# Kernel tuning notes

Hardware: AMD Instinct MI355X
Metric: run time of the kernel (lower is better)

Reference implementation:

```python
import jax, jax.numpy as jnp
import numpy as np

N_NODES = 100000
N_EDGES = 600000
D = 128
BN_EPS = 1e-5


def setup_inputs() -> dict:
    key = jax.random.key(0)
    k1, k2, k3 = jax.random.split(key, 3)
    x = jax.random.normal(k1, (N_NODES, D), dtype=jnp.float32)
    edge_index = jax.random.randint(k2, (2, N_EDGES), 0, N_NODES, dtype=jnp.int64)
    # Linear(in=D, out=D): kaiming-uniform-ish init
    W = jax.random.normal(k3, (D, D), dtype=jnp.float32) / np.sqrt(D)
    b = jnp.zeros((D,), dtype=jnp.float32)
    eps_gin = jnp.zeros((), dtype=jnp.float32)  # train_eps=True, init 0
    gamma = jnp.ones((D,), dtype=jnp.float32)
    beta = jnp.zeros((D,), dtype=jnp.float32)
    return {"x": x, "edge_index": edge_index, "W": W, "b": b,
            "eps_gin": eps_gin, "gamma": gamma, "beta": beta}


def reference(x, edge_index, W, b, eps_gin, gamma, beta):
    src, dst = edge_index[0], edge_index[1]
    # GIN aggregation: sum of source features into destination nodes
    agg = jax.ops.segment_sum(x[src], dst, num_segments=N_NODES)  # [N, D]
    h = (1.0 + eps_gin) * x + agg
    # MLP([D, D]) == single Linear (PyG plain_last)
    h = jnp.einsum('nd,df->nf', h, W.T) + b  # torch Linear: h @ W^T + b
    # BatchNorm1d in training mode (batch stats, biased variance)
    mean = jnp.mean(h, axis=0)
    var = jnp.mean((h - mean) ** 2, axis=0)
    h = (h - mean) * jax.lax.rsqrt(var + BN_EPS) * gamma + beta
    h = jax.nn.relu(h)
    # residual
    return h + x
```

## Files before the change

kernel.cpp:

```cpp
#include <hip/hip_runtime.h>
#include <hip/hip_bf16.h>

#define N_NODES 100000
#define N_EDGES 600000
#define D 128
#define BN_EPS 1e-5f
#define CAP 32
#define NAGG_BLOCKS 1024
#define GEMM_BLOCKS 1024
#define GEMM_NSLOTS (GEMM_BLOCKS * 2)
#define FILL_BLOCKS ((N_EDGES + 255) / 256)

typedef __bf16 bf16x8 __attribute__((ext_vector_type(8)));
typedef float floatx4 __attribute__((ext_vector_type(4)));
typedef unsigned short ushortx8 __attribute__((ext_vector_type(8)));

__device__ __forceinline__ unsigned short f2bf(float f) {
    union { float f; unsigned u; } v; v.f = f;
    unsigned u = v.u;
    unsigned r = u + 0x7FFFu + ((u >> 16) & 1u);
    return (unsigned short)(r >> 16);
}
__device__ __forceinline__ float bflo(unsigned u) {
    union { unsigned u; float f; } v; v.u = u << 16; return v.f;
}
__device__ __forceinline__ float bfhi(unsigned u) {
    union { unsigned u; float f; } v; v.u = u & 0xFFFF0000u; return v.f;
}

__global__ __launch_bounds__(256) void k_fill_gemm(const int* __restrict__ ei,
                                                   int* __restrict__ cursor,
                                                   int* __restrict__ bucket,
                                                   const float* __restrict__ x,
                                                   const float* __restrict__ W,
                                                   unsigned short* __restrict__ y) {
    if (blockIdx.x >= GEMM_BLOCKS) {
        int e = (blockIdx.x - GEMM_BLOCKS) * 256 + threadIdx.x;
        if (e < N_EDGES) {
            int src = ei[e];
            int dst = ei[N_EDGES + e];
            int pos = atomicAdd(&cursor[dst], 1);
            if (pos < CAP) bucket[dst * CAP + pos] = src;
        }
        return;
    }

    const int lane = threadIdx.x & 63;
    const int wid  = threadIdx.x >> 6;
    const int gw   = blockIdx.x * 4 + wid;
    const int fhalf = gw & 1;
    const int pair  = gw >> 1;
    const int n16  = lane & 15;
    const int quad = lane >> 4;
    const int fbase = fhalf * 64;

    bf16x8 B[4][4];
#pragma unroll
    for (int ft = 0; ft < 4; ++ft) {
#pragma unroll
        for (int ks = 0; ks < 4; ++ks) {
            const float* wp = W + (fbase + ft * 16 + n16) * D + ks * 32 + quad * 8;
            float4 wa = *(const float4*)wp;
            float4 wb = *(const float4*)(wp + 4);
            ushortx8 u;
            u[0] = f2bf(wa.x); u[1] = f2bf(wa.y); u[2] = f2bf(wa.z); u[3] = f2bf(wa.w);
            u[4] = f2bf(wb.x); u[5] = f2bf(wb.y); u[6] = f2bf(wb.z); u[7] = f2bf(wb.w);
            B[ft][ks] = __builtin_bit_cast(bf16x8, u);
        }
    }

    for (int chunk = pair; chunk < N_NODES / 16; chunk += GEMM_NSLOTS) {
        const int rbase = chunk * 16;
        floatx4 acc[4];
#pragma unroll
        for (int ft = 0; ft < 4; ++ft) acc[ft] = (floatx4){0.f, 0.f, 0.f, 0.f};

#pragma unroll
        for (int ks = 0; ks < 4; ++ks) {
            const float* xp = x + (size_t)(rbase + n16) * D + ks * 32 + quad * 8;
            float4 xa = *(const float4*)xp;
            float4 xb4 = *(const float4*)(xp + 4);
            ushortx8 u;
            u[0] = f2bf(xa.x); u[1] = f2bf(xa.y); u[2] = f2bf(xa.z); u[3] = f2bf(xa.w);
            u[4] = f2bf(xb4.x); u[5] = f2bf(xb4.y); u[6] = f2bf(xb4.z); u[7] = f2bf(xb4.w);
            bf16x8 a = __builtin_bit_cast(bf16x8, u);
#pragma unroll
            for (int ft = 0; ft < 4; ++ft)
                acc[ft] = __builtin_amdgcn_mfma_f32_16x16x32_bf16(a, B[ft][ks], acc[ft], 0, 0, 0);
        }

#pragma unroll
        for (int ft = 0; ft < 4; ++ft) {
            const int col = fbase + ft * 16 + n16;
#pragma unroll
            for (int i = 0; i < 4; ++i)
                y[(size_t)(rbase + quad * 4 + i) * D + col] = f2bf(acc[ft][i]);
        }
    }
}

__global__ __launch_bounds__(256) void k_agg_y(const int* __restrict__ cursor,
                                               const int* __restrict__ bucket,
                                               const unsigned short* __restrict__ y,
                                               const float* __restrict__ epsp,
                                               unsigned short* __restrict__ zb,
                                               float* __restrict__ pscr) {
    const int t = threadIdx.x;
    const int lane = t & 31;
    const int slot = t >> 5;
    const float one_eps = 1.0f + epsp[0];

    float psum[4] = {0.f, 0.f, 0.f, 0.f};
    float psq[4]  = {0.f, 0.f, 0.f, 0.f};

    for (int base = blockIdx.x * 8; base < N_NODES; base += NAGG_BLOCKS * 8) {
        const int node = base + slot;
        int deg = cursor[node];
        if (deg > CAP) deg = CAP;
        const int* bk = bucket + node * CAP;

        float4 a0 = make_float4(0.f, 0.f, 0.f, 0.f);
        float4 a1 = a0, a2 = a0, a3 = a0, a4 = a0, a5 = a0, a6 = a0, a7 = a0;

        for (int i = 0; i < deg; i += 8) {
            int rem = deg - i, last = rem - 1;
            int s0 = bk[i];
            int s1 = bk[i + (1 < rem ? 1 : last)];
            int s2 = bk[i + (2 < rem ? 2 : last)];
            int s3 = bk[i + (3 < rem ? 3 : last)];
            int s4 = bk[i + (4 < rem ? 4 : last)];
            int s5 = bk[i + (5 < rem ? 5 : last)];
            int s6 = bk[i + (6 < rem ? 6 : last)];
            int s7 = bk[i + (7 < rem ? 7 : last)];
            uint2 v0 = ((const uint2*)(y + (size_t)s0 * D))[lane];
            uint2 v1 = ((const uint2*)(y + (size_t)s1 * D))[lane];
            uint2 v2 = ((const uint2*)(y + (size_t)s2 * D))[lane];
            uint2 v3 = ((const uint2*)(y + (size_t)s3 * D))[lane];
            uint2 v4 = ((const uint2*)(y + (size_t)s4 * D))[lane];
            uint2 v5 = ((const uint2*)(y + (size_t)s5 * D))[lane];
            uint2 v6 = ((const uint2*)(y + (size_t)s6 * D))[lane];
            uint2 v7 = ((const uint2*)(y + (size_t)s7 * D))[lane];
            a0.x += bflo(v0.x); a0.y += bfhi(v0.x); a0.z += bflo(v0.y); a0.w += bfhi(v0.y);
            if (1 < rem) { a1.x += bflo(v1.x); a1.y += bfhi(v1.x); a1.z += bflo(v1.y); a1.w += bfhi(v1.y); }
            if (2 < rem) { a2.x += bflo(v2.x); a2.y += bfhi(v2.x); a2.z += bflo(v2.y); a2.w += bfhi(v2.y); }
            if (3 < rem) { a3.x += bflo(v3.x); a3.y += bfhi(v3.x); a3.z += bflo(v3.y); a3.w += bfhi(v3.y); }
            if (4 < rem) { a4.x += bflo(v4.x); a4.y += bfhi(v4.x); a4.z += bflo(v4.y); a4.w += bfhi(v4.y); }
            if (5 < rem) { a5.x += bflo(v5.x); a5.y += bfhi(v5.x); a5.z += bflo(v5.y); a5.w += bfhi(v5.y); }
            if (6 < rem) { a6.x += bflo(v6.x); a6.y += bfhi(v6.x); a6.z += bflo(v6.y); a6.w += bfhi(v6.y); }
            if (7 < rem) { a7.x += bflo(v7.x); a7.y += bfhi(v7.x); a7.z += bflo(v7.y); a7.w += bfhi(v7.y); }
        }
        float r0 = ((a0.x + a1.x) + (a2.x + a3.x)) + ((a4.x + a5.x) + (a6.x + a7.x));
        float r1 = ((a0.y + a1.y) + (a2.y + a3.y)) + ((a4.y + a5.y) + (a6.y + a7.y));
        float r2 = ((a0.z + a1.z) + (a2.z + a3.z)) + ((a4.z + a5.z) + (a6.z + a7.z));
        float r3 = ((a0.w + a1.w) + (a2.w + a3.w)) + ((a4.w + a5.w) + (a6.w + a7.w));

        uint2 yv = ((const uint2*)(y + (size_t)node * D))[lane];
        float z0 = one_eps * bflo(yv.x) + r0;
        float z1 = one_eps * bfhi(yv.x) + r1;
        float z2 = one_eps * bflo(yv.y) + r2;
        float z3 = one_eps * bfhi(yv.y) + r3;

        ushort4 o;
        o.x = f2bf(z0); o.y = f2bf(z1); o.z = f2bf(z2); o.w = f2bf(z3);
        ((ushort4*)(zb + (size_t)node * D))[lane] = o;

        psum[0] += z0; psq[0] += z0 * z0;
        psum[1] += z1; psq[1] += z1 * z1;
        psum[2] += z2; psq[2] += z2 * z2;
        psum[3] += z3; psq[3] += z3 * z3;
    }

    __shared__ float sred[8][32][8];
#pragma unroll
    for (int j = 0; j < 4; ++j) {
        sred[slot][lane][j]     = psum[j];
        sred[slot][lane][4 + j] = psq[j];
    }
    __syncthreads();
    {
        const int c = t & 127;
        const int j = (t < 128) ? (c & 3) : 4 + (c & 3);
        const int l = c >> 2;
        float acc = 0.f;
#pragma unroll
        for (int s = 0; s < 8; ++s)
            acc += sred[s][l][j];
        pscr[(size_t)blockIdx.x * 256 + t] = acc;
    }
}

__global__ __launch_bounds__(256) void k_bnreduce(const float* __restrict__ pscr,
                                                  float* __restrict__ part2) {
    const int t = threadIdx.x;
    const int b = blockIdx.x;
    float acc = 0.f;
    const float* p = pscr + (size_t)b * (NAGG_BLOCKS / 32) * 256 + t;
#pragma unroll 8
    for (int s = 0; s < NAGG_BLOCKS / 32; ++s)
        acc += p[(size_t)s * 256];
    part2[b * 256 + t] = acc;
}

__global__ __launch_bounds__(256) void k_final(const unsigned short* __restrict__ zb,
                                               const float* __restrict__ x,
                                               const float* __restrict__ part2,
                                               const float* __restrict__ gamma,
                                               const float* __restrict__ beta,
                                               float* __restrict__ out) {
    __shared__ float red[256];
    __shared__ float scs[128], shs[128];
    const int t = threadIdx.x;
    {
        float acc = 0.f;
#pragma unroll 8
        for (int j = 0; j < 32; ++j)
            acc += part2[j * 256 + t];
        red[t] = acc;
    }
    __syncthreads();
    if (t < 128) {
        const float inv_n = 1.0f / (float)N_NODES;
        float mean = red[t] * inv_n;
        float var  = red[128 + t] * inv_n - mean * mean;
        float s    = gamma[t] * rsqrtf(var + BN_EPS);
        scs[t] = s;
        shs[t] = beta[t] - mean * s;
    }
    __syncthreads();

    for (size_t i = (size_t)blockIdx.x * 256 + t; i < (size_t)N_NODES * D / 4;
         i += (size_t)gridDim.x * 256) {
        const size_t idx = i * 4;
        const int f = (int)(idx & (D - 1));
        uint2 zv = *(const uint2*)(zb + idx);
        float4 xv = *(const float4*)(x + idx);
        float z0 = bflo(zv.x), z1 = bfhi(zv.x), z2 = bflo(zv.y), z3 = bfhi(zv.y);
        float4 o;
        o.x = fmaxf(z0 * scs[f]     + shs[f],     0.f) + xv.x;
        o.y = fmaxf(z1 * scs[f + 1] + shs[f + 1], 0.f) + xv.y;
        o.z = fmaxf(z2 * scs[f + 2] + shs[f + 2], 0.f) + xv.z;
        o.w = fmaxf(z3 * scs[f + 3] + shs[f + 3], 0.f) + xv.w;
        *(float4*)(out + idx) = o;
    }
}

extern "C" void kernel_launch(void* const* d_in, const int* in_sizes, int n_in,
                              void* d_out, int out_size, void* d_ws, size_t ws_size,
                              hipStream_t stream) {
    const float* x     = (const float*)d_in[0];
    const int*   ei    = (const int*)d_in[1];
    const float* W     = (const float*)d_in[2];
    const float* epsp  = (const float*)d_in[4];
    const float* gamma = (const float*)d_in[5];
    const float* beta  = (const float*)d_in[6];
    float* out = (float*)d_out;

    char* ws = (char*)d_ws;
    int*   cursor = (int*)ws;
    int*   bucket = (int*)(ws + 400000ull);
    unsigned short* y  = (unsigned short*)(ws + 13200000ull);
    unsigned short* zb = (unsigned short*)(ws + 38800000ull);
    float* pscr  = (float*)(ws + 64400000ull);
    float* part2 = (float*)ws;

    hipMemsetAsync(cursor, 0, 400000ull, stream);

    k_fill_gemm<<<GEMM_BLOCKS + FILL_BLOCKS, 256, 0, stream>>>(ei, cursor, bucket, x, W, y);
    k_agg_y<<<NAGG_BLOCKS, 256, 0, stream>>>(cursor, bucket, y, epsp, zb, pscr);
    k_bnreduce<<<32, 256, 0, stream>>>(pscr, part2);
    k_final<<<2048, 256, 0, stream>>>(zb, x, part2, gamma, beta, out);
}
```

Before: 223.0 us.

## Fuse BN reduction into aggregation via last-block counter and merge fill into GEMM blocks

The separate BN reduction kernel is removed. The last aggregation block to finish, found through an atomic counter, now reduces all partials and writes the scale and shift, so the final kernel just loads them. Edge bucketing now runs on dedicated waves inside 512-thread GEMM blocks using grid-stride loops, in place of separate fill blocks. The aggregation grid is doubled. This cuts one launch and some redundant per-block reduction, but leaves a serial single-block tail over 2048 partials.

```diff
diff --git a/kernel.cpp b/kernel.cpp
--- a/kernel.cpp
+++ b/kernel.cpp
@@ -6,10 +6,10 @@
 #define D 128
 #define BN_EPS 1e-5f
 #define CAP 32
-#define NAGG_BLOCKS 1024
-#define GEMM_BLOCKS 1024
-#define GEMM_NSLOTS (GEMM_BLOCKS * 2)
-#define FILL_BLOCKS ((N_EDGES + 255) / 256)
+#define NAGG_BLOCKS 2048
+#define MEGA_BLOCKS 1024
+#define MEGA_NPAIRS (MEGA_BLOCKS * 3)
+#define EDGE_THREADS (MEGA_BLOCKS * 128)
 
 typedef __bf16 bf16x8 __attribute__((ext_vector_type(8)));
 typedef float floatx4 __attribute__((ext_vector_type(4)));
@@ -28,15 +28,17 @@
     union { unsigned u; float f; } v; v.u = u & 0xFFFF0000u; return v.f;
 }
 
-__global__ __launch_bounds__(256) void k_fill_gemm(const int* __restrict__ ei,
-                                                   int* __restrict__ cursor,
-                                                   int* __restrict__ bucket,
-                                                   const float* __restrict__ x,
-                                                   const float* __restrict__ W,
-                                                   unsigned short* __restrict__ y) {
-    if (blockIdx.x >= GEMM_BLOCKS) {
-        int e = (blockIdx.x - GEMM_BLOCKS) * 256 + threadIdx.x;
-        if (e < N_EDGES) {
+__global__ __launch_bounds__(512) void k_mega(const int* __restrict__ ei,
+                                              int* __restrict__ cursor,
+                                              int* __restrict__ bucket,
+                                              const float* __restrict__ x,
+                                              const float* __restrict__ W,
+                                              unsigned short* __restrict__ y) {
+    const int wid = threadIdx.x >> 6;
+
+    if (wid >= 6) {
+        const int gidx = blockIdx.x * 128 + (threadIdx.x - 384);
+        for (int e = gidx; e < N_EDGES; e += EDGE_THREADS) {
             int src = ei[e];
             int dst = ei[N_EDGES + e];
             int pos = atomicAdd(&cursor[dst], 1);
@@ -46,8 +48,7 @@
     }
 
     const int lane = threadIdx.x & 63;
-    const int wid  = threadIdx.x >> 6;
-    const int gw   = blockIdx.x * 4 + wid;
+    const int gw   = blockIdx.x * 6 + wid;
     const int fhalf = gw & 1;
     const int pair  = gw >> 1;
     const int n16  = lane & 15;
@@ -69,7 +70,7 @@
         }
     }
 
-    for (int chunk = pair; chunk < N_NODES / 16; chunk += GEMM_NSLOTS) {
+    for (int chunk = pair; chunk < N_NODES / 16; chunk += MEGA_NPAIRS) {
         const int rbase = chunk * 16;
         floatx4 acc[4];
 #pragma unroll
@@ -103,8 +104,12 @@
                                                const int* __restrict__ bucket,
                                                const unsigned short* __restrict__ y,
                                                const float* __restrict__ epsp,
+                                               const float* __restrict__ gamma,
+                                               const float* __restrict__ beta,
                                                unsigned short* __restrict__ zb,
-                                               float* __restrict__ pscr) {
+                                               float* __restrict__ pscr,
+                                               int* __restrict__ ctr,
+                                               float* __restrict__ scsh) {
     const int t = threadIdx.x;
     const int lane = t & 31;
     const int slot = t >> 5;
@@ -187,45 +192,42 @@
             acc += sred[s][l][j];
         pscr[(size_t)blockIdx.x * 256 + t] = acc;
     }
-}
-
-__global__ __launch_bounds__(256) void k_bnreduce(const float* __restrict__ pscr,
-                                                  float* __restrict__ part2) {
-    const int t = threadIdx.x;
-    const int b = blockIdx.x;
-    float acc = 0.f;
-    const float* p = pscr + (size_t)b * (NAGG_BLOCKS / 32) * 256 + t;
-#pragma unroll 8
-    for (int s = 0; s < NAGG_BLOCKS / 32; ++s)
-        acc += p[(size_t)s * 256];
-    part2[b * 256 + t] = acc;
+
+    __threadfence();
+    __syncthreads();
+    __shared__ int lastdone;
+    if (t == 0) lastdone = (atomicAdd(ctr, 1) == NAGG_BLOCKS - 1) ? 1 : 0;
+    __syncthreads();
+    if (lastdone) {
+        __threadfence();
+        float acc = 0.f;
+        for (int r = 0; r < NAGG_BLOCKS; r += 8) {
+#pragma unroll
+            for (int rr = 0; rr < 8; ++rr)
+                acc += pscr[(size_t)(r + rr) * 256 + t];
+        }
+        __shared__ float red[256];
+        red[t] = acc;
+        __syncthreads();
+        if (t < 128) {
+            const float inv_n = 1.0f / (float)N_NODES;
+            float mean = red[t] * inv_n;
+            float var  = red[128 + t] * inv_n - mean * mean;
+            float s    = gamma[t] * rsqrtf(var + BN_EPS);
+            scsh[t]       = s;
+            scsh[128 + t] = beta[t] - mean * s;
+        }
+    }
 }
 
 __global__ __launch_bounds__(256) void k_final(const unsigned short* __restrict__ zb,
                                                const float* __restrict__ x,
-                                               const float* __restrict__ part2,
-                                               const float* __restrict__ gamma,
-                                               const float* __restrict__ beta,
+                                               const float* __restrict__ scsh,
                                                float* __restrict__ out) {
-    __shared__ float red[256];
     __shared__ float scs[128], shs[128];
     const int t = threadIdx.x;
-    {
-        float acc = 0.f;
-#pragma unroll 8
-        for (int j = 0; j < 32; ++j)
-            acc += part2[j * 256 + t];
-        red[t] = acc;
-    }
-    __syncthreads();
-    if (t < 128) {
-        const float inv_n = 1.0f / (float)N_NODES;
-        float mean = red[t] * inv_n;
-        float var  = red[128 + t] * inv_n - mean * mean;
-        float s    = gamma[t] * rsqrtf(var + BN_EPS);
-        scs[t] = s;
-        shs[t] = beta[t] - mean * s;
-    }
+    if (t < 128) scs[t] = scsh[t];
+    else         shs[t - 128] = scsh[t];
     __syncthreads();
 
     for (size_t i = (size_t)blockIdx.x * 256 + t; i < (size_t)N_NODES * D / 4;
@@ -257,16 +259,17 @@
 
     char* ws = (char*)d_ws;
     int*   cursor = (int*)ws;
-    int*   bucket = (int*)(ws + 400000ull);
-    unsigned short* y  = (unsigned short*)(ws + 13200000ull);
-    unsigned short* zb = (unsigned short*)(ws + 38800000ull);
-    float* pscr  = (float*)(ws + 64400000ull);
-    float* part2 = (float*)ws;
-
-    hipMemsetAsync(cursor, 0, 400000ull, stream);
-
-    k_fill_gemm<<<GEMM_BLOCKS + FILL_BLOCKS, 256, 0, stream>>>(ei, cursor, bucket, x, W, y);
-    k_agg_y<<<NAGG_BLOCKS, 256, 0, stream>>>(cursor, bucket, y, epsp, zb, pscr);
-    k_bnreduce<<<32, 256, 0, stream>>>(pscr, part2);
-    k_final<<<2048, 256, 0, stream>>>(zb, x, part2, gamma, beta, out);
-}
+    int*   ctr    = (int*)(ws + 400000ull);
+    int*   bucket = (int*)(ws + 400128ull);
+    unsigned short* y  = (unsigned short*)(ws + 13200128ull);
+    unsigned short* zb = (unsigned short*)(ws + 38800128ull);
+    float* pscr = (float*)(ws + 64400128ull);
+    float* scsh = (float*)(ws + 66497280ull);
+
+    hipMemsetAsync(ws, 0, 400128ull, stream);
+
+    k_mega<<<MEGA_BLOCKS, 512, 0, stream>>>(ei, cursor, bucket, x, W, y);
+    k_agg_y<<<NAGG_BLOCKS, 256, 0, stream>>>(cursor, bucket, y, epsp, gamma, beta,
+                                             zb, pscr, ctr, scsh);
+    k_final<<<2048, 256, 0, stream>>>(zb, x, scsh, out);
+}
```

Measured after the change: 480.0 us. 2.15x slower.
